# Kernel optimization log

Hardware: AMD Instinct MI355X
Metric: run time of the kernel (lower is better)

## Reference

```python
import jax, jax.numpy as jnp
import numpy as np

B, C, H, W = 8, 512, 32, 32
N = H * W
FG_THRES, BG_THRES, TOPK = 0.7, 0.6, 12


def setup_inputs() -> dict:
    key = jax.random.key(0)
    k1, k2, k3 = jax.random.split(key, 3)
    feature_q = jax.random.normal(k1, (B, C, H, W), dtype=jnp.float32)
    support_feat = jax.random.normal(k2, (B, C, H, W), dtype=jnp.float32)
    support_mask = jax.random.randint(k3, (B, H, W), 0, 2).astype(jnp.int32)
    return {"feature_q": feature_q, "support_feat": support_feat, "support_mask": support_mask}


def _masked_avg_pool(feat, mask):
    # feat [B,C,H,W], mask [B,1,H,W]; interpolate to same size is identity
    return jnp.sum(feat * mask, axis=(2, 3)) / (jnp.sum(mask, axis=(2, 3)) + 1e-5)


def _cosine(a, b):
    # F.cosine_similarity along channel dim 1 (eps=1e-8), with broadcasting
    dot = jnp.sum(a * b, axis=1)
    na = jnp.sqrt(jnp.sum(a * a, axis=1))
    nb = jnp.sqrt(jnp.sum(b * b, axis=1))
    return dot / jnp.maximum(na * nb, 1e-8)


def _similarity(feature_q, fg_proto, bg_proto):
    sim_fg = _cosine(feature_q, fg_proto)
    sim_bg = _cosine(feature_q, bg_proto)
    return jnp.stack([sim_bg, sim_fg], axis=1) * 10.0  # [B,2,H,W]


def _select_weights(pred, thres):
    # pred [N] -> float {0,1} selection weights; threshold mask, topk-12 fallback
    m = pred > thres
    _, top_idx = jax.lax.top_k(pred, TOPK)
    tm = jnp.zeros_like(m).at[top_idx].set(True)
    return jnp.where(m.sum() > 0, m, tm).astype(pred.dtype)


def _ssp_single(cur_feat, pred_fg, pred_bg):
    # cur_feat [C,N]; masked formulation == torch's variable-length column select
    wf = _select_weights(pred_fg, FG_THRES)
    wb = _select_weights(pred_bg, BG_THRES)
    fg_proto = jnp.sum(cur_feat * wf, axis=-1) / wf.sum()  # [C]
    bg_proto = jnp.sum(cur_feat * wb, axis=-1) / wb.sum()
    cn = cur_feat / jnp.sqrt(jnp.sum(cur_feat * cur_feat, axis=0, keepdims=True))
    sim = (cn.T @ cn) * 2.0  # [N,N] cosine sim, scaled
    neg = jnp.asarray(-1e30, sim.dtype)
    fg_attn = jax.nn.softmax(jnp.where(wf[None, :] > 0, sim, neg), axis=-1)
    bg_attn = jax.nn.softmax(jnp.where(wb[None, :] > 0, sim, neg), axis=-1)
    fg_local = (fg_attn @ cur_feat.T).T  # [C,N]
    bg_local = (bg_attn @ cur_feat.T).T
    return fg_proto, bg_proto, fg_local, bg_local


def reference(feature_q, support_feat, support_mask):
    mask_f = (support_mask == 1).astype(feature_q.dtype)[:, None]  # [B,1,H,W]
    mask_b = (support_mask == 0).astype(feature_q.dtype)[:, None]
    FP = _masked_avg_pool(support_feat, mask_f)[:, :, None, None]  # [B,C,1,1]
    BP = _masked_avg_pool(support_feat, mask_b)[:, :, None, None]
    out_0 = _similarity(feature_q, FP, BP)  # [B,2,H,W]
    pred = jax.nn.softmax(out_0, axis=1).reshape(B, 2, N)
    cur = feature_q.reshape(B, C, N)
    fg_p, bg_p, fg_l, bg_l = jax.vmap(_ssp_single)(cur, pred[:, 1], pred[:, 0])
    SSFP = fg_p[:, :, None, None]
    SSBP = bg_p[:, :, None, None]
    ASBP = bg_l.reshape(B, C, H, W)
    FP_1 = FP * 0.5 + SSFP * 0.5
    BP_1 = SSBP * 0.3 + ASBP * 0.7
    out_1 = _similarity(feature_q, FP_1, BP_1)  # [B,2,H,W]
    return out_1
```

## Files before the change

### kernel.cpp

```cpp
#include <hip/hip_runtime.h>
#include <math.h>

#define Bsz 8
#define Cch 512
#define Npx 1024
#define TOPK 12

typedef __attribute__((ext_vector_type(8))) short bf16x8;
typedef __attribute__((ext_vector_type(4))) float f32x4;

__device__ __forceinline__ unsigned short f2bf(float x) {
    unsigned u = __float_as_uint(x);
    u += 0x7FFF + ((u >> 16) & 1);
    return (unsigned short)(u >> 16);
}
__device__ __forceinline__ float bf2f(unsigned short h) {
    return __uint_as_float(((unsigned)h) << 16);
}

__device__ __forceinline__ float warp_sum64(float v) {
    for (int o = 32; o > 0; o >>= 1) v += __shfl_down(v, o);
    return v;
}
__device__ __forceinline__ float block_sum256(float v, float* s4) {
    v = warp_sum64(v);
    int lane = threadIdx.x & 63, w = threadIdx.x >> 6;
    __syncthreads();
    if (lane == 0) s4[w] = v;
    __syncthreads();
    return s4[0] + s4[1] + s4[2] + s4[3];
}
__device__ __forceinline__ float block_sum512(float v, float* s8) {
    v = warp_sum64(v);
    int lane = threadIdx.x & 63, w = threadIdx.x >> 6;
    __syncthreads();
    if (lane == 0) s8[w] = v;
    __syncthreads();
    float r = 0.f;
    #pragma unroll
    for (int k = 0; k < 8; k++) r += s8[k];
    return r;
}

__global__ void k_pool(const float* __restrict__ sf, const int* __restrict__ mask,
                       float* __restrict__ FPo, float* __restrict__ BPo) {
    __shared__ float s4[4];
    int c = blockIdx.x, b = blockIdx.y, t = threadIdx.x;
    const float4* f4 = (const float4*)(sf + ((size_t)b * Cch + c) * Npx);
    const int4* m4 = (const int4*)(mask + (size_t)b * Npx);
    float4 v = f4[t];
    int4 m = m4[t];
    float sumf = (m.x == 1 ? v.x : 0.f) + (m.y == 1 ? v.y : 0.f)
               + (m.z == 1 ? v.z : 0.f) + (m.w == 1 ? v.w : 0.f);
    float tot = v.x + v.y + v.z + v.w;
    float cf = (float)((m.x == 1) + (m.y == 1) + (m.z == 1) + (m.w == 1));
    sumf = block_sum256(sumf, s4);
    tot  = block_sum256(tot, s4);
    cf   = block_sum256(cf, s4);
    if (t == 0) {
        FPo[b * Cch + c] = sumf / (cf + 1e-5f);
        BPo[b * Cch + c] = (tot - sumf) / ((1024.f - cf) + 1e-5f);
    }
}

__global__ void __launch_bounds__(512) k_predcast(const float* __restrict__ fq,
                       const float* __restrict__ FP, const float* __restrict__ BP,
                       float* __restrict__ dsim, float* __restrict__ invn,
                       unsigned short* __restrict__ Ft, float* __restrict__ denom) {
    __shared__ float sFP[Cch], sBP[Cch], s8[8];
    __shared__ float rdf[16][32], rdb[16][32], rqq[16][32];
    __shared__ unsigned short S[32][522];
    int b = blockIdx.y, t = threadIdx.x;
    int tx = t & 31, ty = t >> 5;
    int p0 = blockIdx.x * 32;
    int p = p0 + tx;
    if (t < 32) denom[b * Npx + p0 + t] = 0.f;
    sFP[t] = FP[b * Cch + t];
    sBP[t] = BP[b * Cch + t];
    __syncthreads();
    float nf = sqrtf(block_sum512(sFP[t] * sFP[t], s8));
    float nb = sqrtf(block_sum512(sBP[t] * sBP[t], s8));
    const float* q = fq + (size_t)b * Cch * Npx + p;
    float df = 0.f, db = 0.f, qq = 0.f;
    int c0 = ty * 32;
    #pragma unroll 4
    for (int c = 0; c < 32; c += 2) {
        float v0 = q[(size_t)(c0 + c) * Npx];
        float v1 = q[(size_t)(c0 + c + 1) * Npx];
        df += v0 * sFP[c0 + c] + v1 * sFP[c0 + c + 1];
        db += v0 * sBP[c0 + c] + v1 * sBP[c0 + c + 1];
        qq += v0 * v0 + v1 * v1;
        unsigned pk = (unsigned)f2bf(v0) | ((unsigned)f2bf(v1) << 16);
        *(unsigned*)&S[tx][c0 + c] = pk;
    }
    rdf[ty][tx] = df; rdb[ty][tx] = db; rqq[ty][tx] = qq;
    __syncthreads();
    for (int s = 8; s > 0; s >>= 1) {
        if (ty < s) {
            rdf[ty][tx] += rdf[ty + s][tx];
            rdb[ty][tx] += rdb[ty + s][tx];
            rqq[ty][tx] += rqq[ty + s][tx];
        }
        __syncthreads();
    }
    if (ty == 0) {
        float nq = sqrtf(rqq[0][tx]);
        float simf = 10.f * rdf[0][tx] / fmaxf(nq * nf, 1e-8f);
        float simb = 10.f * rdb[0][tx] / fmaxf(nq * nb, 1e-8f);
        dsim[b * Npx + p] = simf - simb;
        invn[b * Npx + p] = 1.f / nq;
    }
    int w = t >> 6, lane = t & 63;
    unsigned short* FtB = Ft + (size_t)b * Npx * Cch;
    for (int pr = w; pr < 32; pr += 8) {
        unsigned* dst = (unsigned*)(FtB + (size_t)(p0 + pr) * Cch);
        #pragma unroll
        for (int it = 0; it < 4; it++) {
            int d = it * 64 + lane;
            dst[d] = *(const unsigned*)&S[pr][d * 2];
        }
    }
}

__global__ void __launch_bounds__(1024) k_selcompact(const float* __restrict__ dsim,
                        const float* __restrict__ invn,
                        int* __restrict__ nsf, int* __restrict__ nsb,
                        int* __restrict__ jf, int* __restrict__ jb,
                        float* __restrict__ ivg) {
    __shared__ int wsum[16];
    int b = blockIdx.y, t = threadIdx.x;
    int lane = t & 63, w = t >> 6;
    bool isf = (blockIdx.x == 0);
    float d = dsim[b * Npx + t];
    float key = isf ? d : -d;
    float thres = isf ? 0.8472979f : 0.4054651f;
    int flag = (key > thres) ? 1 : 0;
    int x = flag;
    #pragma unroll
    for (int o = 1; o < 64; o <<= 1) {
        int y = __shfl_up(x, o);
        if (lane >= o) x += y;
    }
    if (lane == 63) wsum[w] = x;
    __syncthreads();
    int base = 0, total = 0;
    #pragma unroll
    for (int k = 0; k < 16; k++) {
        int s = wsum[k];
        if (k < w) base += s;
        total += s;
    }
    if (total == 0) {
        __shared__ int   sc[Npx];
        __shared__ float v[Npx];
        __shared__ float rv[Npx];
        __shared__ int   ri[Npx];
        v[t] = key; flag = 0;
        __syncthreads();
        for (int k = 0; k < TOPK; k++) {
            rv[t] = v[t]; ri[t] = t;
            __syncthreads();
            for (int s = 512; s > 0; s >>= 1) {
                if (t < s) {
                    float a = rv[t], bb = rv[t + s];
                    int ia = ri[t], ib = ri[t + s];
                    if (bb > a || (bb == a && ib < ia)) { rv[t] = bb; ri[t] = ib; }
                }
                __syncthreads();
            }
            int win = ri[0];
            if (t == win) { flag = 1; v[t] = -INFINITY; }
            __syncthreads();
        }
        sc[t] = flag;
        __syncthreads();
        for (int off = 1; off < 1024; off <<= 1) {
            int xx = (t >= off) ? sc[t - off] : 0;
            __syncthreads();
            sc[t] += xx;
            __syncthreads();
        }
        if (flag) {
            int pos = sc[t] - 1;
            if (isf) jf[b * Npx + pos] = t;
            else {
                jb[b * Npx + pos] = t;
                ivg[b * Npx + pos] = invn[b * Npx + t];
            }
        }
        if (t == 1023) { if (isf) nsf[b] = sc[1023]; else nsb[b] = sc[1023]; }
        return;
    }
    if (flag) {
        int pos = base + x - 1;
        if (isf) jf[b * Npx + pos] = t;
        else {
            jb[b * Npx + pos] = t;
            ivg[b * Npx + pos] = invn[b * Npx + t];
        }
    }
    if (t == 0) { if (isf) nsf[b] = total; else nsb[b] = total; }
}

__global__ void k_mid(const float* __restrict__ fq, const unsigned short* __restrict__ Ft,
                      const int* __restrict__ jf, const int* __restrict__ nsf,
                      const int* __restrict__ jb, const int* __restrict__ nsb,
                      unsigned short* __restrict__ Fg,
                      float* __restrict__ fgp, float* __restrict__ bgp) {
    int b = blockIdx.z;
    if (blockIdx.y < 16) {
        int ns = nsb[b];
        int KC = (ns + 31) & ~31;
        int j0 = blockIdx.x * 32;
        if (j0 >= KC) return;
        int c0 = blockIdx.y * 32;
        __shared__ unsigned short tt[32][33];
        int col = threadIdx.x & 31, rr = threadIdx.x >> 5;
        const unsigned short* S = Ft + (size_t)b * Npx * Cch;
        const int* ji = jb + b * Npx;
        for (int r = rr; r < 32; r += 8) {
            int j = j0 + r;
            int src = (j < ns) ? ji[j] : ji[ns - 1];
            tt[r][col] = S[(size_t)src * Cch + c0 + col];
        }
        __syncthreads();
        unsigned short* D = Fg + (size_t)b * Cch * Npx;
        for (int r = rr; r < 32; r += 8)
            D[(size_t)(c0 + r) * Npx + j0 + col] = tt[col][r];
    } else {
        if (blockIdx.x >= 16) return;
        int cb = blockIdx.x * 32;
        int tx = threadIdx.x & 31, ty = threadIdx.x >> 5;
        const float* F = fq + (size_t)b * Cch * Npx;
        for (int which = 0; which < 2; which++) {
            const int* ji = (which ? jb : jf) + b * Npx;
            int ns = (which ? nsb : nsf)[b];
            for (int g = 0; g < 4; g++) {
                int c = cb + g * 8 + ty;
                float s = 0.f;
                for (int k = tx; k < ns; k += 32) s += F[(size_t)c * Npx + ji[k]];
                #pragma unroll
                for (int o = 16; o > 0; o >>= 1) s += __shfl_down(s, o);
                if (tx == 0) (which ? bgp : fgp)[b * Cch + c] = s / (float)ns;
            }
        }
    }
}

__global__ void __launch_bounds__(256) k_gram_fused(const unsigned short* __restrict__ Ft,
                        const int* __restrict__ jb, const int* __restrict__ nsb,
                        const float* __restrict__ invn, const float* __restrict__ ivg,
                        unsigned short* __restrict__ G, float* __restrict__ denom) {
    int b = blockIdx.z;
    int ns = nsb[b];
    int KC = (ns + 31) & ~31;
    int j0 = blockIdx.y * 64;
    if (j0 >= KC) return;
    int i0 = blockIdx.x * 128;
    __shared__ unsigned short At[128][40];
    __shared__ unsigned short Bt[64][40];
    __shared__ int sji[64];
    __shared__ float sfi[128], sfj[64];
    const unsigned short* FA = Ft + (size_t)b * Npx * Cch;
    int tid = threadIdx.x;
    if (tid < 64) {
        int j = j0 + tid;
        sji[tid] = (j < ns) ? jb[b * Npx + j] : jb[b * Npx];
        sfj[tid] = (j < ns) ? ivg[b * Npx + j] : 0.f;
    }
    if (tid < 128) sfi[tid] = 2.f * invn[b * Npx + i0 + tid];
    __syncthreads();
    int rA = tid >> 2, kc8 = (tid & 3) * 8;
    const unsigned short* sa0 = FA + (size_t)(i0 + rA) * Cch + kc8;
    const unsigned short* sa1 = sa0 + (size_t)64 * Cch;
    const unsigned short* sb0 = FA + (size_t)sji[rA] * Cch + kc8;
    unsigned short* wa0 = &At[rA][kc8];
    unsigned short* wa1 = &At[64 + rA][kc8];
    unsigned short* wb0 = &Bt[rA][kc8];
    int l = tid & 63, w = tid >> 6;
    int ml = l & 15, quad = l >> 4;
    int wi = (w & 1) * 64, wj = (w >> 1) * 32;
    f32x4 acc[4][2] = {};
    uint4 a0 = *(const uint4*)sa0;
    uint4 a1 = *(const uint4*)sa1;
    uint4 b0 = *(const uint4*)sb0;
    for (int k0 = 0; k0 < Cch; k0 += 32) {
        __syncthreads();
        *(uint4*)wa0 = a0; *(uint4*)wa1 = a1; *(uint4*)wb0 = b0;
        __syncthreads();
        int kn = k0 + 32;
        if (kn < Cch) {
            a0 = *(const uint4*)(sa0 + kn);
            a1 = *(const uint4*)(sa1 + kn);
            b0 = *(const uint4*)(sb0 + kn);
        }
        bf16x8 af[4], bfr[2];
        #pragma unroll
        for (int u = 0; u < 4; u++) af[u] = *(const bf16x8*)&At[wi + u * 16 + ml][quad * 8];
        #pragma unroll
        for (int v = 0; v < 2; v++) bfr[v] = *(const bf16x8*)&Bt[wj + v * 16 + ml][quad * 8];
        #pragma unroll
        for (int u = 0; u < 4; u++)
            #pragma unroll
            for (int v = 0; v < 2; v++)
                acc[u][v] = __builtin_amdgcn_mfma_f32_16x16x32_bf16(af[u], bfr[v], acc[u][v], 0, 0, 0);
    }
    unsigned short* g = G + (size_t)b * Npx * Npx;
    float* dn = denom + b * Npx;
    #pragma unroll
    for (int u = 0; u < 4; u++) {
        int il = wi + u * 16 + quad * 4;
        #pragma unroll
        for (int r = 0; r < 4; r++) {
            float fi = sfi[il + r];
            float s = 0.f;
            #pragma unroll
            for (int v = 0; v < 2; v++) {
                int jl = wj + v * 16 + ml;
                float e = 0.f;
                if (j0 + jl < ns) e = expf(acc[u][v][r] * fi * sfj[jl]);
                unsigned short eb = f2bf(e);
                g[(size_t)(i0 + il + r) * Npx + j0 + jl] = eb;
                s += bf2f(eb);
            }
            #pragma unroll
            for (int m = 1; m < 16; m <<= 1) s += __shfl_xor(s, m);
            if (ml == 0) atomicAdd(&dn[i0 + il + r], s);
        }
    }
}

__global__ void __launch_bounds__(256) k_pv_c(const unsigned short* __restrict__ Fg,
                                              const unsigned short* __restrict__ A,
                                              const int* __restrict__ nsb,
                                              const float* __restrict__ denom,
                                              unsigned short* __restrict__ Dout) {
    int b = blockIdx.z;
    int KC = (nsb[b] + 31) & ~31;
    __shared__ unsigned short At[64][40];
    __shared__ unsigned short Bt[128][40];
    int i0 = blockIdx.x * 128, c0 = blockIdx.y * 64;
    const unsigned short* F = Fg + (size_t)b * Cch * Npx;
    const unsigned short* Ar = A + (size_t)b * Npx * Npx;
    int tid = threadIdx.x;
    int rr = tid >> 2, kc8 = (tid & 3) * 8;
    const unsigned short* sa0 = F + (size_t)(c0 + rr) * Npx + kc8;
    const unsigned short* sb0 = Ar + (size_t)(i0 + rr) * Npx + kc8;
    const unsigned short* sb1 = sb0 + (size_t)64 * Npx;
    unsigned short* wa0 = &At[rr][kc8];
    unsigned short* wb0 = &Bt[rr][kc8];
    unsigned short* wb1 = &Bt[64 + rr][kc8];
    int l = tid & 63, w = tid >> 6;
    int ml = l & 15, quad = l >> 4;
    int wm = (w & 1) * 32, wn = (w >> 1) * 64;
    f32x4 acc[2][4] = {};
    uint4 a0 = *(const uint4*)sa0;
    uint4 b0 = *(const uint4*)sb0;
    uint4 b1 = *(const uint4*)sb1;
    for (int j0 = 0; j0 < KC; j0 += 32) {
        __syncthreads();
        *(uint4*)wa0 = a0; *(uint4*)wb0 = b0; *(uint4*)wb1 = b1;
        __syncthreads();
        int jn = j0 + 32;
        if (jn < KC) {
            a0 = *(const uint4*)(sa0 + jn);
            b0 = *(const uint4*)(sb0 + jn);
            b1 = *(const uint4*)(sb1 + jn);
        }
        bf16x8 af[2], bfr[4];
        #pragma unroll
        for (int u = 0; u < 2; u++) af[u] = *(const bf16x8*)&At[wm + u * 16 + ml][quad * 8];
        #pragma unroll
        for (int v = 0; v < 4; v++) bfr[v] = *(const bf16x8*)&Bt[wn + v * 16 + ml][quad * 8];
        #pragma unroll
        for (int u = 0; u < 2; u++)
            #pragma unroll
            for (int v = 0; v < 4; v++)
                acc[u][v] = __builtin_amdgcn_mfma_f32_16x16x32_bf16(af[u], bfr[v], acc[u][v], 0, 0, 0);
    }
    float rd[4];
    #pragma unroll
    for (int v = 0; v < 4; v++) rd[v] = 1.f / denom[b * Npx + i0 + wn + v * 16 + ml];
    unsigned short* D = Dout + (size_t)b * Cch * Npx;
    #pragma unroll
    for (int u = 0; u < 2; u++) {
        int c = c0 + wm + u * 16 + quad * 4;
        #pragma unroll
        for (int v = 0; v < 4; v++) {
            int i = i0 + wn + v * 16 + ml;
            #pragma unroll
            for (int r = 0; r < 4; r++)
                D[(size_t)(c + r) * Npx + i] = f2bf(acc[u][v][r] * rd[v]);
        }
    }
}

__global__ void __launch_bounds__(512) k_out(const unsigned short* __restrict__ Ft,
                      const float* __restrict__ FP,
                      const float* __restrict__ fgp, const float* __restrict__ bgp,
                      const unsigned short* __restrict__ localh, float* __restrict__ out) {
    __shared__ float sFP1[Cch], sBG[Cch], s8[8];
    __shared__ float rdf[16][32], rdb[16][32], rqq[16][32], rnb[16][32];
    int b = blockIdx.y, t = threadIdx.x;
    int tx = t & 31, ty = t >> 5;
    int p = blockIdx.x * 32 + tx;
    sFP1[t] = 0.5f * FP[b * Cch + t] + 0.5f * fgp[b * Cch + t];
    sBG[t] = 0.3f * bgp[b * Cch + t];
    __syncthreads();
    float nf = sqrtf(block_sum512(sFP1[t] * sFP1[t], s8));
    const unsigned short* qr = Ft + ((size_t)b * Npx + p) * Cch;
    const unsigned short* lo = localh + (size_t)b * Cch * Npx + p;
    float df = 0.f, db = 0.f, qq = 0.f, nb2 = 0.f;
    int c0 = ty * 32;
    #pragma unroll
    for (int cc = 0; cc < 4; cc++) {
        bf16x8 qv = *(const bf16x8*)&qr[c0 + cc * 8];
        #pragma unroll
        for (int e = 0; e < 8; e++) {
            int c = c0 + cc * 8 + e;
            float v = bf2f((unsigned short)qv[e]);
            float bp1 = sBG[c] + 0.7f * bf2f(lo[(size_t)c * Npx]);
            df += v * sFP1[c];
            db += v * bp1;
            qq += v * v;
            nb2 += bp1 * bp1;
        }
    }
    rdf[ty][tx] = df; rdb[ty][tx] = db; rqq[ty][tx] = qq; rnb[ty][tx] = nb2;
    __syncthreads();
    for (int s = 8; s > 0; s >>= 1) {
        if (ty < s) {
            rdf[ty][tx] += rdf[ty + s][tx];
            rdb[ty][tx] += rdb[ty + s][tx];
            rqq[ty][tx] += rqq[ty + s][tx];
            rnb[ty][tx] += rnb[ty + s][tx];
        }
        __syncthreads();
    }
    if (ty == 0) {
        float nq = sqrtf(rqq[0][tx]);
        float sf = 10.f * rdf[0][tx] / fmaxf(nq * nf, 1e-8f);
        float sb = 10.f * rdb[0][tx] / fmaxf(nq * sqrtf(rnb[0][tx]), 1e-8f);
        out[((size_t)b * 2) * Npx + p] = sb;
        out[((size_t)b * 2 + 1) * Npx + p] = sf;
    }
}

extern "C" void kernel_launch(void* const* d_in, const int* in_sizes, int n_in,
                              void* d_out, int out_size, void* d_ws, size_t ws_size,
                              hipStream_t stream) {
    const float* fq = (const float*)d_in[0];
    const float* sf = (const float*)d_in[1];
    const int* mask = (const int*)d_in[2];
    float* out = (float*)d_out;

    float* ws = (float*)d_ws;
    float* FP    = ws;
    float* BP    = FP + Bsz * Cch;
    float* fgp   = BP + Bsz * Cch;
    float* bgp   = fgp + Bsz * Cch;
    float* dsim  = bgp + Bsz * Cch;
    float* invn  = dsim + Bsz * Npx;
    float* ivg   = invn + Bsz * Npx;
    int*   nsf   = (int*)(ivg + Bsz * Npx);
    int*   nsb   = nsf + 8;
    int*   jf    = nsb + 8;
    int*   jb    = jf + Bsz * Npx;
    unsigned short* Ft     = (unsigned short*)(jb + Bsz * Npx);
    unsigned short* Fg     = Ft + (size_t)Bsz * Npx * Cch;
    unsigned short* Gb     = Fg + (size_t)Bsz * Cch * Npx;
    unsigned short* localh = Gb + (size_t)Bsz * Npx * Npx;
    float* denom = (float*)(localh + (size_t)Bsz * Cch * Npx);

    k_pool<<<dim3(Cch, Bsz), 256, 0, stream>>>(sf, mask, FP, BP);
    k_predcast<<<dim3(Npx / 32, Bsz), 512, 0, stream>>>(fq, FP, BP, dsim, invn, Ft, denom);
    k_selcompact<<<dim3(2, Bsz), 1024, 0, stream>>>(dsim, invn, nsf, nsb, jf, jb, ivg);
    k_mid<<<dim3(32, 17, Bsz), 256, 0, stream>>>(fq, Ft, jf, nsf, jb, nsb, Fg, fgp, bgp);
    k_gram_fused<<<dim3(8, 16, Bsz), 256, 0, stream>>>(Ft, jb, nsb, invn, ivg, Gb, denom);
    k_pv_c<<<dim3(8, 8, Bsz), 256, 0, stream>>>(Fg, Gb, nsb, denom, localh);
    k_out<<<dim3(Npx / 32, Bsz), 512, 0, stream>>>(Ft, FP, fgp, bgp, localh, out);
}
```

Measured before the change: 153.8 us.

## Fold k_mid into selcompact and gram kernels, shrink GEMM tiles to 64x64

Removes the k_mid launch. The fg/bg prototype sums now run inside k_selcompact, reading the bf16 transposed features gathered by the compacted indices. The Fg gather/transpose runs as extra blocks of k_gram_fused. Both GEMM kernels (gram and PV) drop to 64x64 output tiles with one 16-row strip per wave, which doubles the block count for better occupancy on small batches. The trade-offs are that prototypes are now summed from bf16 instead of fp32, and each block gets less data reuse.

```diff
diff --git a/kernel.cpp b/kernel.cpp
--- a/kernel.cpp
+++ b/kernel.cpp
@@ -124,10 +124,14 @@
 
 __global__ void __launch_bounds__(1024) k_selcompact(const float* __restrict__ dsim,
                         const float* __restrict__ invn,
+                        const unsigned short* __restrict__ Ft,
                         int* __restrict__ nsf, int* __restrict__ nsb,
                         int* __restrict__ jf, int* __restrict__ jb,
-                        float* __restrict__ ivg) {
+                        float* __restrict__ ivg,
+                        float* __restrict__ fgp, float* __restrict__ bgp) {
     __shared__ int wsum[16];
+    __shared__ int sns;
+    __shared__ float sProto[16][512];
     int b = blockIdx.y, t = threadIdx.x;
     int lane = t & 63, w = t >> 6;
     bool isf = (blockIdx.x == 0);
@@ -150,6 +154,7 @@
         if (k < w) base += s;
         total += s;
     }
+    int* jdst = (isf ? jf : jb) + b * Npx;
     if (total == 0) {
         __shared__ int   sc[Npx];
         __shared__ float v[Npx];
@@ -182,151 +187,135 @@
         }
         if (flag) {
             int pos = sc[t] - 1;
-            if (isf) jf[b * Npx + pos] = t;
-            else {
-                jb[b * Npx + pos] = t;
-                ivg[b * Npx + pos] = invn[b * Npx + t];
-            }
-        }
-        if (t == 1023) { if (isf) nsf[b] = sc[1023]; else nsb[b] = sc[1023]; }
-        return;
-    }
-    if (flag) {
-        int pos = base + x - 1;
-        if (isf) jf[b * Npx + pos] = t;
-        else {
-            jb[b * Npx + pos] = t;
-            ivg[b * Npx + pos] = invn[b * Npx + t];
-        }
-    }
-    if (t == 0) { if (isf) nsf[b] = total; else nsb[b] = total; }
-}
-
-__global__ void k_mid(const float* __restrict__ fq, const unsigned short* __restrict__ Ft,
-                      const int* __restrict__ jf, const int* __restrict__ nsf,
-                      const int* __restrict__ jb, const int* __restrict__ nsb,
-                      unsigned short* __restrict__ Fg,
-                      float* __restrict__ fgp, float* __restrict__ bgp) {
-    int b = blockIdx.z;
-    if (blockIdx.y < 16) {
-        int ns = nsb[b];
-        int KC = (ns + 31) & ~31;
-        int j0 = blockIdx.x * 32;
-        if (j0 >= KC) return;
-        int c0 = blockIdx.y * 32;
-        __shared__ unsigned short tt[32][33];
-        int col = threadIdx.x & 31, rr = threadIdx.x >> 5;
-        const unsigned short* S = Ft + (size_t)b * Npx * Cch;
-        const int* ji = jb + b * Npx;
-        for (int r = rr; r < 32; r += 8) {
-            int j = j0 + r;
-            int src = (j < ns) ? ji[j] : ji[ns - 1];
-            tt[r][col] = S[(size_t)src * Cch + c0 + col];
-        }
-        __syncthreads();
-        unsigned short* D = Fg + (size_t)b * Cch * Npx;
-        for (int r = rr; r < 32; r += 8)
-            D[(size_t)(c0 + r) * Npx + j0 + col] = tt[col][r];
+            jdst[pos] = t;
+            if (!isf) ivg[b * Npx + pos] = invn[b * Npx + t];
+        }
+        if (t == 1023) sns = sc[1023];
     } else {
-        if (blockIdx.x >= 16) return;
-        int cb = blockIdx.x * 32;
-        int tx = threadIdx.x & 31, ty = threadIdx.x >> 5;
-        const float* F = fq + (size_t)b * Cch * Npx;
-        for (int which = 0; which < 2; which++) {
-            const int* ji = (which ? jb : jf) + b * Npx;
-            int ns = (which ? nsb : nsf)[b];
-            for (int g = 0; g < 4; g++) {
-                int c = cb + g * 8 + ty;
-                float s = 0.f;
-                for (int k = tx; k < ns; k += 32) s += F[(size_t)c * Npx + ji[k]];
-                #pragma unroll
-                for (int o = 16; o > 0; o >>= 1) s += __shfl_down(s, o);
-                if (tx == 0) (which ? bgp : fgp)[b * Cch + c] = s / (float)ns;
-            }
-        }
+        if (flag) {
+            int pos = base + x - 1;
+            jdst[pos] = t;
+            if (!isf) ivg[b * Npx + pos] = invn[b * Npx + t];
+        }
+        if (t == 0) sns = total;
+    }
+    __syncthreads();
+    int ns = sns;
+    if (t == 0) (isf ? nsf : nsb)[b] = ns;
+    const unsigned short* FtB = Ft + (size_t)b * Npx * Cch;
+    float facc[8] = {0.f, 0.f, 0.f, 0.f, 0.f, 0.f, 0.f, 0.f};
+    int k = w;
+    int row = (k < ns) ? jdst[k] : 0;
+    while (k < ns) {
+        int kn = k + 16;
+        int rown = (kn < ns) ? jdst[kn] : 0;
+        bf16x8 vv = *(const bf16x8*)&FtB[(size_t)row * Cch + lane * 8];
+        #pragma unroll
+        for (int e = 0; e < 8; e++) facc[e] += bf2f((unsigned short)vv[e]);
+        k = kn; row = rown;
+    }
+    #pragma unroll
+    for (int e = 0; e < 8; e++) sProto[w][lane * 8 + e] = facc[e];
+    __syncthreads();
+    if (t < 512) {
+        float s = 0.f;
+        #pragma unroll
+        for (int q = 0; q < 16; q++) s += sProto[q][t];
+        (isf ? fgp : bgp)[b * Cch + t] = s / (float)ns;
     }
 }
 
 __global__ void __launch_bounds__(256) k_gram_fused(const unsigned short* __restrict__ Ft,
                         const int* __restrict__ jb, const int* __restrict__ nsb,
                         const float* __restrict__ invn, const float* __restrict__ ivg,
-                        unsigned short* __restrict__ G, float* __restrict__ denom) {
+                        unsigned short* __restrict__ G, unsigned short* __restrict__ Fg,
+                        float* __restrict__ denom) {
     int b = blockIdx.z;
     int ns = nsb[b];
     int KC = (ns + 31) & ~31;
+    if (blockIdx.y >= 16) {
+        int j0 = blockIdx.x * 64;
+        if (j0 >= KC) return;
+        int c0 = (blockIdx.y - 16) * 32;
+        __shared__ unsigned short tt[64][34];
+        const unsigned short* S = Ft + (size_t)b * Npx * Cch;
+        const int* ji = jb + b * Npx;
+        int col = threadIdx.x & 31, rr = threadIdx.x >> 5;
+        for (int r = rr; r < 64; r += 8) {
+            int j = j0 + r;
+            int src = (j < ns) ? ji[j] : ji[0];
+            tt[r][col] = S[(size_t)src * Cch + c0 + col];
+        }
+        __syncthreads();
+        unsigned* D32 = (unsigned*)(Fg + (size_t)b * Cch * Npx);
+        int jx = threadIdx.x & 31;
+        for (int cr = rr; cr < 32; cr += 8) {
+            unsigned lo = tt[2 * jx][cr], hi = tt[2 * jx + 1][cr];
+            D32[(size_t)(c0 + cr) * (Npx / 2) + (j0 >> 1) + jx] = lo | (hi << 16);
+        }
+        return;
+    }
     int j0 = blockIdx.y * 64;
     if (j0 >= KC) return;
-    int i0 = blockIdx.x * 128;
-    __shared__ unsigned short At[128][40];
+    int i0 = blockIdx.x * 64;
+    __shared__ unsigned short At[64][40];
     __shared__ unsigned short Bt[64][40];
     __shared__ int sji[64];
-    __shared__ float sfi[128], sfj[64];
+    __shared__ float sfi[64], sfj[64];
     const unsigned short* FA = Ft + (size_t)b * Npx * Cch;
     int tid = threadIdx.x;
     if (tid < 64) {
         int j = j0 + tid;
         sji[tid] = (j < ns) ? jb[b * Npx + j] : jb[b * Npx];
         sfj[tid] = (j < ns) ? ivg[b * Npx + j] : 0.f;
-    }
-    if (tid < 128) sfi[tid] = 2.f * invn[b * Npx + i0 + tid];
+        sfi[tid] = 2.f * invn[b * Npx + i0 + tid];
+    }
     __syncthreads();
     int rA = tid >> 2, kc8 = (tid & 3) * 8;
     const unsigned short* sa0 = FA + (size_t)(i0 + rA) * Cch + kc8;
-    const unsigned short* sa1 = sa0 + (size_t)64 * Cch;
     const unsigned short* sb0 = FA + (size_t)sji[rA] * Cch + kc8;
-    unsigned short* wa0 = &At[rA][kc8];
-    unsigned short* wa1 = &At[64 + rA][kc8];
-    unsigned short* wb0 = &Bt[rA][kc8];
     int l = tid & 63, w = tid >> 6;
     int ml = l & 15, quad = l >> 4;
-    int wi = (w & 1) * 64, wj = (w >> 1) * 32;
-    f32x4 acc[4][2] = {};
+    f32x4 acc[4] = {};
     uint4 a0 = *(const uint4*)sa0;
-    uint4 a1 = *(const uint4*)sa1;
     uint4 b0 = *(const uint4*)sb0;
     for (int k0 = 0; k0 < Cch; k0 += 32) {
         __syncthreads();
-        *(uint4*)wa0 = a0; *(uint4*)wa1 = a1; *(uint4*)wb0 = b0;
+        *(uint4*)&At[rA][kc8] = a0;
+        *(uint4*)&Bt[rA][kc8] = b0;
         __syncthreads();
         int kn = k0 + 32;
         if (kn < Cch) {
             a0 = *(const uint4*)(sa0 + kn);
-            a1 = *(const uint4*)(sa1 + kn);
             b0 = *(const uint4*)(sb0 + kn);
         }
-        bf16x8 af[4], bfr[2];
-        #pragma unroll
-        for (int u = 0; u < 4; u++) af[u] = *(const bf16x8*)&At[wi + u * 16 + ml][quad * 8];
-        #pragma unroll
-        for (int v = 0; v < 2; v++) bfr[v] = *(const bf16x8*)&Bt[wj + v * 16 + ml][quad * 8];
-        #pragma unroll
-        for (int u = 0; u < 4; u++)
-            #pragma unroll
-            for (int v = 0; v < 2; v++)
-                acc[u][v] = __builtin_amdgcn_mfma_f32_16x16x32_bf16(af[u], bfr[v], acc[u][v], 0, 0, 0);
+        bf16x8 af = *(const bf16x8*)&At[w * 16 + ml][quad * 8];
+        bf16x8 bfr[4];
+        #pragma unroll
+        for (int v = 0; v < 4; v++) bfr[v] = *(const bf16x8*)&Bt[v * 16 + ml][quad * 8];
+        #pragma unroll
+        for (int v = 0; v < 4; v++)
+            acc[v] = __builtin_amdgcn_mfma_f32_16x16x32_bf16(af, bfr[v], acc[v], 0, 0, 0);
     }
     unsigned short* g = G + (size_t)b * Npx * Npx;
     float* dn = denom + b * Npx;
     #pragma unroll
-    for (int u = 0; u < 4; u++) {
-        int il = wi + u * 16 + quad * 4;
-        #pragma unroll
-        for (int r = 0; r < 4; r++) {
-            float fi = sfi[il + r];
-            float s = 0.f;
-            #pragma unroll
-            for (int v = 0; v < 2; v++) {
-                int jl = wj + v * 16 + ml;
-                float e = 0.f;
-                if (j0 + jl < ns) e = expf(acc[u][v][r] * fi * sfj[jl]);
-                unsigned short eb = f2bf(e);
-                g[(size_t)(i0 + il + r) * Npx + j0 + jl] = eb;
-                s += bf2f(eb);
-            }
-            #pragma unroll
-            for (int m = 1; m < 16; m <<= 1) s += __shfl_xor(s, m);
-            if (ml == 0) atomicAdd(&dn[i0 + il + r], s);
-        }
+    for (int r = 0; r < 4; r++) {
+        int il = w * 16 + quad * 4 + r;
+        float fi = sfi[il];
+        float s = 0.f;
+        #pragma unroll
+        for (int v = 0; v < 4; v++) {
+            int jl = v * 16 + ml;
+            float e = 0.f;
+            if (j0 + jl < ns) e = expf(acc[v][r] * fi * sfj[jl]);
+            unsigned short eb = f2bf(e);
+            g[(size_t)(i0 + il) * Npx + j0 + jl] = eb;
+            s += bf2f(eb);
+        }
+        #pragma unroll
+        for (int m = 1; m < 16; m <<= 1) s += __shfl_xor(s, m);
+        if (ml == 0) atomicAdd(&dn[i0 + il], s);
     }
 }
 
@@ -338,60 +327,47 @@
     int b = blockIdx.z;
     int KC = (nsb[b] + 31) & ~31;
     __shared__ unsigned short At[64][40];
-    __shared__ unsigned short Bt[128][40];
-    int i0 = blockIdx.x * 128, c0 = blockIdx.y * 64;
+    __shared__ unsigned short Bt[64][40];
+    int i0 = blockIdx.x * 64, c0 = blockIdx.y * 64;
     const unsigned short* F = Fg + (size_t)b * Cch * Npx;
     const unsigned short* Ar = A + (size_t)b * Npx * Npx;
     int tid = threadIdx.x;
     int rr = tid >> 2, kc8 = (tid & 3) * 8;
     const unsigned short* sa0 = F + (size_t)(c0 + rr) * Npx + kc8;
     const unsigned short* sb0 = Ar + (size_t)(i0 + rr) * Npx + kc8;
-    const unsigned short* sb1 = sb0 + (size_t)64 * Npx;
-    unsigned short* wa0 = &At[rr][kc8];
-    unsigned short* wb0 = &Bt[rr][kc8];
-    unsigned short* wb1 = &Bt[64 + rr][kc8];
     int l = tid & 63, w = tid >> 6;
     int ml = l & 15, quad = l >> 4;
-    int wm = (w & 1) * 32, wn = (w >> 1) * 64;
-    f32x4 acc[2][4] = {};
+    f32x4 acc[4] = {};
     uint4 a0 = *(const uint4*)sa0;
     uint4 b0 = *(const uint4*)sb0;
-    uint4 b1 = *(const uint4*)sb1;
     for (int j0 = 0; j0 < KC; j0 += 32) {
         __syncthreads();
-        *(uint4*)wa0 = a0; *(uint4*)wb0 = b0; *(uint4*)wb1 = b1;
+        *(uint4*)&At[rr][kc8] = a0;
+        *(uint4*)&Bt[rr][kc8] = b0;
         __syncthreads();
         int jn = j0 + 32;
         if (jn < KC) {
             a0 = *(const uint4*)(sa0 + jn);
             b0 = *(const uint4*)(sb0 + jn);
-            b1 = *(const uint4*)(sb1 + jn);
-        }
-        bf16x8 af[2], bfr[4];
-        #pragma unroll
-        for (int u = 0; u < 2; u++) af[u] = *(const bf16x8*)&At[wm + u * 16 + ml][quad * 8];
-        #pragma unroll
-        for (int v = 0; v < 4; v++) bfr[v] = *(const bf16x8*)&Bt[wn + v * 16 + ml][quad * 8];
-        #pragma unroll
-        for (int u = 0; u < 2; u++)
-            #pragma unroll
-            for (int v = 0; v < 4; v++)
-                acc[u][v] = __builtin_amdgcn_mfma_f32_16x16x32_bf16(af[u], bfr[v], acc[u][v], 0, 0, 0);
+        }
+        bf16x8 af = *(const bf16x8*)&At[w * 16 + ml][quad * 8];
+        bf16x8 bfr[4];
+        #pragma unroll
+        for (int v = 0; v < 4; v++) bfr[v] = *(const bf16x8*)&Bt[v * 16 + ml][quad * 8];
+        #pragma unroll
+        for (int v = 0; v < 4; v++)
+            acc[v] = __builtin_amdgcn_mfma_f32_16x16x32_bf16(af, bfr[v], acc[v], 0, 0, 0);
     }
     float rd[4];
     #pragma unroll
-    for (int v = 0; v < 4; v++) rd[v] = 1.f / denom[b * Npx + i0 + wn + v * 16 + ml];
+    for (int v = 0; v < 4; v++) rd[v] = 1.f / denom[b * Npx + i0 + v * 16 + ml];
     unsigned short* D = Dout + (size_t)b * Cch * Npx;
     #pragma unroll
-    for (int u = 0; u < 2; u++) {
-        int c = c0 + wm + u * 16 + quad * 4;
-        #pragma unroll
-        for (int v = 0; v < 4; v++) {
-            int i = i0 + wn + v * 16 + ml;
-            #pragma unroll
-            for (int r = 0; r < 4; r++)
-                D[(size_t)(c + r) * Npx + i] = f2bf(acc[u][v][r] * rd[v]);
-        }
+    for (int r = 0; r < 4; r++) {
+        int c = c0 + w * 16 + quad * 4 + r;
+        #pragma unroll
+        for (int v = 0; v < 4; v++)
+            D[(size_t)c * Npx + i0 + v * 16 + ml] = f2bf(acc[v][r] * rd[v]);
     }
 }
 
@@ -474,9 +450,8 @@
 
     k_pool<<<dim3(Cch, Bsz), 256, 0, stream>>>(sf, mask, FP, BP);
     k_predcast<<<dim3(Npx / 32, Bsz), 512, 0, stream>>>(fq, FP, BP, dsim, invn, Ft, denom);
-    k_selcompact<<<dim3(2, Bsz), 1024, 0, stream>>>(dsim, invn, nsf, nsb, jf, jb, ivg);
-    k_mid<<<dim3(32, 17, Bsz), 256, 0, stream>>>(fq, Ft, jf, nsf, jb, nsb, Fg, fgp, bgp);
-    k_gram_fused<<<dim3(8, 16, Bsz), 256, 0, stream>>>(Ft, jb, nsb, invn, ivg, Gb, denom);
-    k_pv_c<<<dim3(8, 8, Bsz), 256, 0, stream>>>(Fg, Gb, nsb, denom, localh);
+    k_selcompact<<<dim3(2, Bsz), 1024, 0, stream>>>(dsim, invn, Ft, nsf, nsb, jf, jb, ivg, fgp, bgp);
+    k_gram_fused<<<dim3(16, 32, Bsz), 256, 0, stream>>>(Ft, jb, nsb, invn, ivg, Gb, Fg, denom);
+    k_pv_c<<<dim3(Npx / 64, Cch / 64, Bsz), 256, 0, stream>>>(Fg, Gb, nsb, denom, localh);
     k_out<<<dim3(Npx / 32, Bsz), 512, 0, stream>>>(Ft, FP, fgp, bgp, localh, out);
 }
```

Measured after the change: 134.3 us. 1.14x faster.
